# Kernel tuning notes

Measured on AMD Instinct MI355X. Metric: run time of the kernel, lower is better.

## Reference

```python
import jax, jax.numpy as jnp
import numpy as np

B, I, O = 512, 1024, 1024

def setup_inputs() -> dict:
    key = jax.random.key(0)
    kx, kw = jax.random.split(key)
    x = jax.random.normal(kx, (B, I), dtype=jnp.float32)
    W = jax.random.normal(kw, (O, I), dtype=jnp.float32)
    return {"x": x, "W": W}

def reference(x, W):
    # Tropical (max-plus) linear map: y[b, o] = max_i (x[b, i] + W[o, i])
    # Faithful to the torch broadcast-add + max-reduce formulation.
    out = x[..., None, :] + W[None, :, :]  # [B, O, I]
    return jnp.max(out, axis=-1)           # [B, O]
```

## Files before the change

kernel.cpp:

```cpp
#include <hip/hip_runtime.h>
#include <float.h>


#define B_DIM 512
#define I_DIM 1024
#define O_DIM 1024
#define BT 128
#define OT 128
#define KT 16

__device__ __forceinline__ void g2lds16(const float* g, float* l) {
    __builtin_amdgcn_global_load_lds(
        (const __attribute__((address_space(1))) void*)g,
        (__attribute__((address_space(3))) void*)l, 16, 0, 0);
}

template <int KB>
__global__ __launch_bounds__(256, 2) void trop_main(
    const float* __restrict__ xT,
    const float* __restrict__ wT,
    float* __restrict__ part)
{
    constexpr int NCH = KB / KT;
    static_assert(KB % KT == 0, "");
    __shared__ __align__(16) float xs[2][KT * BT];
    __shared__ __align__(16) float ws[2][KT * OT];

    const int tid  = threadIdx.x;
    const int to   = tid & 15;
    const int tb   = tid >> 4;
    const int wave = tid >> 6;
    const int lane = tid & 63;
    const int o0 = blockIdx.x * OT;
    const int b0 = blockIdx.y * BT;
    const int kz = blockIdx.z;
    const int kbase = kz * KB;

    const int rk = lane >> 5;
    const int cb = (lane & 31) * 4;

    float acc[8][8];
    #pragma unroll
    for (int i = 0; i < 8; ++i)
        #pragma unroll
        for (int j = 0; j < 8; ++j)
            acc[i][j] = -FLT_MAX;

    auto stage = [&](int c, int buf) {
        const int k0 = kbase + c * KT;
        #pragma unroll
        for (int i = 0; i < 2; ++i) {
            const int t = wave * 2 + i;
            g2lds16(&xT[(size_t)(k0 + 2 * t + rk) * B_DIM + b0 + cb],
                    &xs[buf][t * 256]);
        }
        #pragma unroll
        for (int i = 0; i < 2; ++i) {
            const int t = wave * 2 + i;
            g2lds16(&wT[(size_t)(k0 + 2 * t + rk) * O_DIM + o0 + cb],
                    &ws[buf][t * 256]);
        }
    };

    auto compute = [&](int buf) {
        const float* xB = &xs[buf][4 * tb];
        const float* wB = &ws[buf][4 * to];
        #pragma unroll
        for (int k = 0; k < KT; k += 2) {
            const float4 xa0 = *(const float4*)&xB[k * BT];
            const float4 xa1 = *(const float4*)&xB[k * BT + 64];
            const float4 xb0 = *(const float4*)&xB[(k + 1) * BT];
            const float4 xb1 = *(const float4*)&xB[(k + 1) * BT + 64];
            const float4 wa0 = *(const float4*)&wB[k * OT];
            const float4 wa1 = *(const float4*)&wB[k * OT + 64];
            const float4 wb0 = *(const float4*)&wB[(k + 1) * OT];
            const float4 wb1 = *(const float4*)&wB[(k + 1) * OT + 64];

            const float xa[8] = {xa0.x, xa0.y, xa0.z, xa0.w, xa1.x, xa1.y, xa1.z, xa1.w};
            const float xb[8] = {xb0.x, xb0.y, xb0.z, xb0.w, xb1.x, xb1.y, xb1.z, xb1.w};
            const float wa[8] = {wa0.x, wa0.y, wa0.z, wa0.w, wa1.x, wa1.y, wa1.z, wa1.w};
            const float wb[8] = {wb0.x, wb0.y, wb0.z, wb0.w, wb1.x, wb1.y, wb1.z, wb1.w};

            #pragma unroll
            for (int i = 0; i < 8; ++i)
                #pragma unroll
                for (int j = 0; j < 8; ++j) {
                    const float s0 = xa[i] + wa[j];
                    const float s1 = xb[i] + wb[j];
                    acc[i][j] = fmaxf(acc[i][j], fmaxf(s0, s1));
                }
        }
    };

    stage(0, 0);
    #pragma unroll
    for (int c = 0; c < NCH; ++c) {
        __syncthreads();
        if (c + 1 < NCH) stage(c + 1, (c + 1) & 1);
        compute(c & 1);
    }

    float* pout = part + (size_t)kz * (B_DIM * O_DIM);
    #pragma unroll
    for (int i = 0; i < 8; ++i) {
        const int b = b0 + (i >> 2) * 64 + 4 * tb + (i & 3);
        float4 v0 = make_float4(acc[i][0], acc[i][1], acc[i][2], acc[i][3]);
        float4 v1 = make_float4(acc[i][4], acc[i][5], acc[i][6], acc[i][7]);
        *(float4*)&pout[(size_t)b * O_DIM + o0 + 4 * to]      = v0;
        *(float4*)&pout[(size_t)b * O_DIM + o0 + 64 + 4 * to] = v1;
    }
}

__global__ __launch_bounds__(256) void transpose3(
    const float* __restrict__ x, float* __restrict__ xT,
    const float* __restrict__ W, float* __restrict__ wT)
{
    __shared__ float tile[32][33];
    const int tx = threadIdx.x;
    const int ty = threadIdx.y;
    const int z  = blockIdx.z;
    const float* in; float* out; int dst_ld;
    if (z == 0) { in = x;                  out = xT;            dst_ld = B_DIM; }
    else        { in = W + (z - 1) * 512 * I_DIM;
                  out = wT + (z - 1) * 512;                     dst_ld = O_DIM; }
    const int r0 = blockIdx.y * 32;
    const int c0 = blockIdx.x * 32;
    #pragma unroll
    for (int i = 0; i < 4; ++i)
        tile[ty + 8 * i][tx] = in[(size_t)(r0 + ty + 8 * i) * I_DIM + c0 + tx];
    __syncthreads();
    #pragma unroll
    for (int i = 0; i < 4; ++i)
        out[(size_t)(c0 + ty + 8 * i) * dst_ld + r0 + tx] = tile[tx][ty + 8 * i];
}

template <int KS>
__global__ __launch_bounds__(256) void trop_reduce(
    const float* __restrict__ part, float* __restrict__ y)
{
    constexpr int N4 = B_DIM * O_DIM / 4;
    const int idx = blockIdx.x * 256 + threadIdx.x;
    const float4* p = (const float4*)part;
    float4 m = p[idx];
    #pragma unroll
    for (int s = 1; s < KS; ++s) {
        const float4 v = p[(size_t)s * N4 + idx];
        m.x = fmaxf(m.x, v.x); m.y = fmaxf(m.y, v.y);
        m.z = fmaxf(m.z, v.z); m.w = fmaxf(m.w, v.w);
    }
    ((float4*)y)[idx] = m;
}

__global__ __launch_bounds__(256) void trop_naive(
    const float* __restrict__ x, const float* __restrict__ W,
    float* __restrict__ y)
{
    const int idx = blockIdx.x * 256 + threadIdx.x;
    const int b = idx / O_DIM, o = idx % O_DIM;
    float m = -FLT_MAX;
    for (int i = 0; i < I_DIM; ++i)
        m = fmaxf(m, x[b * I_DIM + i] + W[o * I_DIM + i]);
    y[idx] = m;
}

extern "C" void kernel_launch(void* const* d_in, const int* in_sizes, int n_in,
                              void* d_out, int out_size, void* d_ws, size_t ws_size,
                              hipStream_t stream) {
    const float* x = (const float*)d_in[0];
    const float* W = (const float*)d_in[1];
    float* y = (float*)d_out;

    const size_t slab  = (size_t)B_DIM * O_DIM * sizeof(float);
    const size_t xT_sz = (size_t)B_DIM * I_DIM * sizeof(float);
    const size_t wT_sz = (size_t)O_DIM * I_DIM * sizeof(float);
    const dim3 rgrid(B_DIM * O_DIM / 4 / 256);
    const dim3 tgrid(I_DIM / 32, 512 / 32, 3);
    const dim3 tblk(32, 8);

    if (ws_size >= 16 * slab + xT_sz + wT_sz) {
        float* part = (float*)d_ws;
        float* xT = part + 16 * (B_DIM * O_DIM);
        float* wT = xT + B_DIM * I_DIM;
        transpose3<<<tgrid, tblk, 0, stream>>>(x, xT, W, wT);
        trop_main<I_DIM / 16><<<dim3(O_DIM / OT, B_DIM / BT, 16), 256, 0, stream>>>(xT, wT, part);
        trop_reduce<16><<<rgrid, 256, 0, stream>>>(part, y);
    } else if (ws_size >= 8 * slab + xT_sz + wT_sz) {
        float* part = (float*)d_ws;
        float* xT = part + 8 * (B_DIM * O_DIM);
        float* wT = xT + B_DIM * I_DIM;
        transpose3<<<tgrid, tblk, 0, stream>>>(x, xT, W, wT);
        trop_main<I_DIM / 8><<<dim3(O_DIM / OT, B_DIM / BT, 8), 256, 0, stream>>>(xT, wT, part);
        trop_reduce<8><<<rgrid, 256, 0, stream>>>(part, y);
    } else if (ws_size >= xT_sz + wT_sz) {
        float* xT = (float*)d_ws;
        float* wT = xT + B_DIM * I_DIM;
        transpose3<<<tgrid, tblk, 0, stream>>>(x, xT, W, wT);
        trop_main<I_DIM><<<dim3(O_DIM / OT, B_DIM / BT, 1), 256, 0, stream>>>(xT, wT, y);
    } else {
        trop_naive<<<dim3(B_DIM * O_DIM / 256), 256, 0, stream>>>(x, W, y);
    }
}
```

Baseline: 89.77 us.

## Give each wave a private LDS tile to drop block-wide barriers

The main tropical kernel now gives each wave its own LDS slices: 32 batch rows of x plus a full private copy of the 128-column W tile. Each wave stages only its own data, so the per-chunk __syncthreads is removed and waves no longer stall on each other. The K chunk shrinks from 16 to 8 so the duplicated W buffers still fit in LDS. The cost is four times the W traffic from L2 into LDS, a larger LDS footprint, and a reliance on the compiler placing waits correctly for the async global-to-LDS loads now that no barrier forces them. A few size_t casts on index arithmetic are also added.

```diff
diff --git a/kernel.cpp b/kernel.cpp
--- a/kernel.cpp
+++ b/kernel.cpp
@@ -7,7 +7,7 @@
 #define O_DIM 1024
 #define BT 128
 #define OT 128
-#define KT 16
+#define KT 8
 
 __device__ __forceinline__ void g2lds16(const float* g, float* l) {
     __builtin_amdgcn_global_load_lds(
@@ -23,21 +23,24 @@
 {
     constexpr int NCH = KB / KT;
     static_assert(KB % KT == 0, "");
-    __shared__ __align__(16) float xs[2][KT * BT];
-    __shared__ __align__(16) float ws[2][KT * OT];
+    __shared__ __align__(16) float xs[4][2][KT * 32];
+    __shared__ __align__(16) float ws[4][2][KT * 128];
 
     const int tid  = threadIdx.x;
-    const int to   = tid & 15;
-    const int tb   = tid >> 4;
     const int wave = tid >> 6;
     const int lane = tid & 63;
+    const int to   = lane & 15;
+    const int tbw  = lane >> 4;
     const int o0 = blockIdx.x * OT;
     const int b0 = blockIdx.y * BT;
+    const int bw0 = b0 + 32 * wave;
     const int kz = blockIdx.z;
     const int kbase = kz * KB;
 
-    const int rk = lane >> 5;
-    const int cb = (lane & 31) * 4;
+    const int rk8 = lane >> 3;
+    const int xc4 = (lane & 7) * 4;
+    const int rk2 = lane >> 5;
+    const int wc4 = (lane & 31) * 4;
 
     float acc[8][8];
     #pragma unroll
@@ -48,33 +51,27 @@
 
     auto stage = [&](int c, int buf) {
         const int k0 = kbase + c * KT;
+        g2lds16(&xT[(size_t)(k0 + rk8) * B_DIM + bw0 + xc4],
+                &xs[wave][buf][0]);
         #pragma unroll
-        for (int i = 0; i < 2; ++i) {
-            const int t = wave * 2 + i;
-            g2lds16(&xT[(size_t)(k0 + 2 * t + rk) * B_DIM + b0 + cb],
-                    &xs[buf][t * 256]);
-        }
-        #pragma unroll
-        for (int i = 0; i < 2; ++i) {
-            const int t = wave * 2 + i;
-            g2lds16(&wT[(size_t)(k0 + 2 * t + rk) * O_DIM + o0 + cb],
-                    &ws[buf][t * 256]);
-        }
+        for (int t = 0; t < 4; ++t)
+            g2lds16(&wT[(size_t)(k0 + 2 * t + rk2) * O_DIM + o0 + wc4],
+                    &ws[wave][buf][t * 256]);
     };
 
     auto compute = [&](int buf) {
-        const float* xB = &xs[buf][4 * tb];
-        const float* wB = &ws[buf][4 * to];
+        const float* xB = &xs[wave][buf][4 * tbw];
+        const float* wB = &ws[wave][buf][4 * to];
         #pragma unroll
         for (int k = 0; k < KT; k += 2) {
-            const float4 xa0 = *(const float4*)&xB[k * BT];
-            const float4 xa1 = *(const float4*)&xB[k * BT + 64];
-            const float4 xb0 = *(const float4*)&xB[(k + 1) * BT];
-            const float4 xb1 = *(const float4*)&xB[(k + 1) * BT + 64];
-            const float4 wa0 = *(const float4*)&wB[k * OT];
-            const float4 wa1 = *(const float4*)&wB[k * OT + 64];
-            const float4 wb0 = *(const float4*)&wB[(k + 1) * OT];
-            const float4 wb1 = *(const float4*)&wB[(k + 1) * OT + 64];
+            const float4 xa0 = *(const float4*)&xB[k * 32];
+            const float4 xa1 = *(const float4*)&xB[k * 32 + 16];
+            const float4 xb0 = *(const float4*)&xB[(k + 1) * 32];
+            const float4 xb1 = *(const float4*)&xB[(k + 1) * 32 + 16];
+            const float4 wa0 = *(const float4*)&wB[k * 128];
+            const float4 wa1 = *(const float4*)&wB[k * 128 + 64];
+            const float4 wb0 = *(const float4*)&wB[(k + 1) * 128];
+            const float4 wb1 = *(const float4*)&wB[(k + 1) * 128 + 64];
 
             const float xa[8] = {xa0.x, xa0.y, xa0.z, xa0.w, xa1.x, xa1.y, xa1.z, xa1.w};
             const float xb[8] = {xb0.x, xb0.y, xb0.z, xb0.w, xb1.x, xb1.y, xb1.z, xb1.w};
@@ -95,7 +92,6 @@
     stage(0, 0);
     #pragma unroll
     for (int c = 0; c < NCH; ++c) {
-        __syncthreads();
         if (c + 1 < NCH) stage(c + 1, (c + 1) & 1);
         compute(c & 1);
     }
@@ -103,7 +99,7 @@
     float* pout = part + (size_t)kz * (B_DIM * O_DIM);
     #pragma unroll
     for (int i = 0; i < 8; ++i) {
-        const int b = b0 + (i >> 2) * 64 + 4 * tb + (i & 3);
+        const int b = bw0 + (i >> 2) * 16 + 4 * tbw + (i & 3);
         float4 v0 = make_float4(acc[i][0], acc[i][1], acc[i][2], acc[i][3]);
         float4 v1 = make_float4(acc[i][4], acc[i][5], acc[i][6], acc[i][7]);
         *(float4*)&pout[(size_t)b * O_DIM + o0 + 4 * to]      = v0;
@@ -121,7 +117,7 @@
     const int z  = blockIdx.z;
     const float* in; float* out; int dst_ld;
     if (z == 0) { in = x;                  out = xT;            dst_ld = B_DIM; }
-    else        { in = W + (z - 1) * 512 * I_DIM;
+    else        { in = W + (size_t)(z - 1) * 512 * I_DIM;
                   out = wT + (z - 1) * 512;                     dst_ld = O_DIM; }
     const int r0 = blockIdx.y * 32;
     const int c0 = blockIdx.x * 32;
@@ -179,14 +175,14 @@
 
     if (ws_size >= 16 * slab + xT_sz + wT_sz) {
         float* part = (float*)d_ws;
-        float* xT = part + 16 * (B_DIM * O_DIM);
+        float* xT = part + 16 * (size_t)(B_DIM * O_DIM);
         float* wT = xT + B_DIM * I_DIM;
         transpose3<<<tgrid, tblk, 0, stream>>>(x, xT, W, wT);
         trop_main<I_DIM / 16><<<dim3(O_DIM / OT, B_DIM / BT, 16), 256, 0, stream>>>(xT, wT, part);
         trop_reduce<16><<<rgrid, 256, 0, stream>>>(part, y);
     } else if (ws_size >= 8 * slab + xT_sz + wT_sz) {
         float* part = (float*)d_ws;
-        float* xT = part + 8 * (B_DIM * O_DIM);
+        float* xT = part + 8 * (size_t)(B_DIM * O_DIM);
         float* wT = xT + B_DIM * I_DIM;
         transpose3<<<tgrid, tblk, 0, stream>>>(x, xT, W, wT);
         trop_main<I_DIM / 8><<<dim3(O_DIM / OT, B_DIM / BT, 8), 256, 0, stream>>>(xT, wT, part);
```

After: 88.78 us. No clear change (-1.1%).
